# Kernel tuning notes

Hardware: AMD Instinct MI355X
Metric: run time of the kernel (lower is better)

Reference implementation:

```python
import jax, jax.numpy as jnp
import numpy as np

N_HEADS = 8
DIM = 128
BT, A, M = 2880, 10, 350  # bs*T, agents, map tokens (from forwards())
TOPK_SELF, TOPK_CROSS = 3, 32


def _split_heads(x, h):
    B, T, C = x.shape
    return x.reshape(B, T, h, C // h).transpose(0, 2, 1, 3)  # [B,h,T,hd]


def _biased_attn(q, k, v, pe, rel):
    """flex_attention with score_mod: score + pe[b,q,rel[b,q,kv],h], -inf where rel==-1.
    q:[B,H,Tq,d] k,v:[B,H,Tk,d] pe:[B,Tq,K,H] rel:[B,Tq,Tk] int"""
    d = q.shape[-1]
    scores = jnp.einsum('bhqd,bhkd->bhqk', q, k) / jnp.sqrt(jnp.asarray(d, q.dtype))
    safe = jnp.maximum(rel, 0)
    bias = jnp.take_along_axis(pe, safe[:, :, :, None], axis=2)  # [B,Tq,Tk,H]
    bias = bias.transpose(0, 3, 1, 2)                            # [B,H,Tq,Tk]
    scores = jnp.where(rel[:, None, :, :] > -1, scores + bias, -jnp.inf)
    attn = jax.nn.softmax(scores, axis=-1)
    out = jnp.einsum('bhqk,bhkd->bhqd', attn, v)
    B, H, Tq, hd = out.shape
    return out.transpose(0, 2, 1, 3).reshape(B, Tq, H * hd)


def _make_relation(key, B, Tq, Tk, topk):
    # topk random keys per query get offsets 0..topk-1 in ascending kv order; rest -1
    rand = jax.random.uniform(key, (B, Tq, Tk))
    idx = jnp.sort(jax.lax.top_k(rand, topk)[1], axis=-1)  # [B,Tq,topk]
    rel = jnp.full((B, Tq, Tk), -1, dtype=jnp.int32)
    b = jnp.arange(B)[:, None, None]
    qi = jnp.arange(Tq)[None, :, None]
    return rel.at[b, qi, idx].set(jnp.arange(topk, dtype=jnp.int32)[None, None, :])


def setup_inputs() -> dict:
    key = jax.random.key(0)
    ks = jax.random.split(key, 12)
    s = 0.02
    return {
        'a_token': jax.random.normal(ks[0], (BT, A, DIM), jnp.float32),
        'm_token': jax.random.normal(ks[1], (BT, M, DIM), jnp.float32),
        'a2m_pe': jax.random.uniform(ks[2], (BT, A, TOPK_CROSS, N_HEADS), jnp.float32),
        'a_pe': jax.random.uniform(ks[3], (BT, A, TOPK_SELF, N_HEADS), jnp.float32),
        'Wq': s * jax.random.normal(ks[4], (DIM, DIM), jnp.float32),
        'Wk': s * jax.random.normal(ks[5], (DIM, DIM), jnp.float32),
        'Wv': s * jax.random.normal(ks[6], (DIM, DIM), jnp.float32),
        'W_cross_proj': s * jax.random.normal(ks[7], (DIM, DIM), jnp.float32),
        'W_cattn': s * jax.random.normal(ks[8], (DIM, 3 * DIM), jnp.float32),
        'W_self_proj': s * jax.random.normal(ks[9], (DIM, DIM), jnp.float32),
        'a2m_relation': _make_relation(ks[10], BT, A, M, TOPK_CROSS),
        'a_relation': _make_relation(ks[11], BT, A, A, TOPK_SELF),
    }


def reference(a_token, m_token, a2m_pe, a_pe, Wq, Wk, Wv, W_cross_proj,
              W_cattn, W_self_proj, a2m_relation, a_relation):
    # cross attention: q from a_token, k/v from m_token (dropout=0 => identity)
    q = _split_heads(a_token @ Wq, N_HEADS)
    k = _split_heads(m_token @ Wk, N_HEADS)
    v = _split_heads(m_token @ Wv, N_HEADS)
    y = _biased_attn(q, k, v, a2m_pe, a2m_relation) @ W_cross_proj
    # self attention with fused qkv projection
    q2, k2, v2 = jnp.split(y @ W_cattn, 3, axis=-1)
    y2 = _biased_attn(_split_heads(q2, N_HEADS), _split_heads(k2, N_HEADS),
                      _split_heads(v2, N_HEADS), a_pe, a_relation)
    return y2 @ W_self_proj
```

## Files before the change

kernel.cpp:

```cpp
#include <hip/hip_runtime.h>
#include <hip/hip_bf16.h>


typedef __attribute__((ext_vector_type(4))) float f32x4;
typedef __attribute__((ext_vector_type(8))) short bf16x8v;
typedef __attribute__((ext_vector_type(4))) short short4v;

#define BT_N 2880
#define A_N  10
#define M_N  350
#define BQ_N (BT_N * A_N)
#define DIMC 128

static __device__ __forceinline__ short f2b(float x) {
    __hip_bfloat16 b = __float2bfloat16(x);
    return __builtin_bit_cast(short, b);
}
static __device__ __forceinline__ float b2f(short s) {
    unsigned u = ((unsigned)(unsigned short)s) << 16;
    return __builtin_bit_cast(float, u);
}

__global__ __launch_bounds__(256) void precompute_mats(
    const float* __restrict__ Wq, const float* __restrict__ Wk,
    const float* __restrict__ Wv, const float* __restrict__ Wcp,
    const float* __restrict__ Wc, const float* __restrict__ Wsp,
    short* __restrict__ S1t, short* __restrict__ VP1t,
    short* __restrict__ S2t, short* __restrict__ VP2t)
{
    int gid = blockIdx.x * 256 + threadIdx.x;
    int mat = gid >> 17;
    int idx = gid & 131071;
    float acc = 0.f;
    if (mat == 0) {
        int n = idx >> 7, c = idx & 127;
        int h = n >> 7, d = n & 127;
        #pragma unroll
        for (int t = 0; t < 16; ++t)
            acc += Wq[c * 128 + h * 16 + t] * Wk[d * 128 + h * 16 + t];
        S1t[idx] = f2b(acc * 0.25f);
    } else if (mat == 1) {
        int d = idx >> 10, o = idx & 1023;
        int h = o >> 7, c = o & 127;
        #pragma unroll
        for (int t = 0; t < 16; ++t)
            acc += Wv[c * 128 + h * 16 + t] * Wcp[(h * 16 + t) * 128 + d];
        VP1t[idx] = f2b(acc);
    } else if (mat == 2) {
        int n = idx >> 7, c = idx & 127;
        int h = n >> 7, d = n & 127;
        #pragma unroll
        for (int t = 0; t < 16; ++t)
            acc += Wc[c * 384 + h * 16 + t] * Wc[d * 384 + 128 + h * 16 + t];
        S2t[idx] = f2b(acc * 0.25f);
    } else {
        int d = idx >> 10, o = idx & 1023;
        int h = o >> 7, c = o & 127;
        #pragma unroll
        for (int t = 0; t < 16; ++t)
            acc += Wc[c * 384 + 256 + h * 16 + t] * Wsp[(h * 16 + t) * 128 + d];
        VP2t[idx] = f2b(acc);
    }
}

template<bool AF32, bool CF32>
__global__ __launch_bounds__(256) void gemm_bt(
    const void* __restrict__ Ap, const short* __restrict__ Bt,
    void* __restrict__ Cp, int M, int N, int K)
{
    __shared__ short As[128][72];
    __shared__ short Bs[128][72];
    const int tid  = threadIdx.x;
    const int bm   = blockIdx.y << 7, bn = blockIdx.x << 7;
    const int wave = tid >> 6, lane = tid & 63;
    const int wm   = (wave >> 1) << 6, wn = (wave & 1) << 6;
    const int row16 = lane & 15, kq = (lane >> 4) << 3;
    f32x4 acc[4][4] = {};

    for (int k0 = 0; k0 < K; k0 += 64) {
        if (AF32) {
            const float* A = (const float*)Ap;
            #pragma unroll
            for (int i = 0; i < 8; ++i) {
                int f = (i << 8) + tid;
                int r = f >> 4, c = (f & 15) << 2;
                f32x4 v = *(const f32x4*)(A + (size_t)(bm + r) * K + k0 + c);
                short4v t;
                t.x = f2b(v.x); t.y = f2b(v.y); t.z = f2b(v.z); t.w = f2b(v.w);
                *(short4v*)&As[r][c] = t;
            }
        } else {
            const short* A = (const short*)Ap;
            #pragma unroll
            for (int i = 0; i < 4; ++i) {
                int g = (i << 8) + tid;
                int r = g >> 3, c = (g & 7) << 3;
                *(bf16x8v*)&As[r][c] = *(const bf16x8v*)(A + (size_t)(bm + r) * K + k0 + c);
            }
        }
        #pragma unroll
        for (int i = 0; i < 4; ++i) {
            int g = (i << 8) + tid;
            int r = g >> 3, c = (g & 7) << 3;
            *(bf16x8v*)&Bs[r][c] = *(const bf16x8v*)(Bt + (size_t)(bn + r) * K + k0 + c);
        }
        __syncthreads();
        #pragma unroll
        for (int kk = 0; kk < 64; kk += 32) {
            bf16x8v af[4], bfr[4];
            #pragma unroll
            for (int mi = 0; mi < 4; ++mi)
                af[mi] = *(const bf16x8v*)&As[wm + (mi << 4) + row16][kq + kk];
            #pragma unroll
            for (int ni = 0; ni < 4; ++ni)
                bfr[ni] = *(const bf16x8v*)&Bs[wn + (ni << 4) + row16][kq + kk];
            #pragma unroll
            for (int mi = 0; mi < 4; ++mi)
                #pragma unroll
                for (int ni = 0; ni < 4; ++ni)
                    acc[mi][ni] = __builtin_amdgcn_mfma_f32_16x16x32_bf16(
                        af[mi], bfr[ni], acc[mi][ni], 0, 0, 0);
        }
        __syncthreads();
    }

    const int col = lane & 15, rb = (lane >> 4) << 2;
    #pragma unroll
    for (int mi = 0; mi < 4; ++mi)
        #pragma unroll
        for (int ni = 0; ni < 4; ++ni)
            #pragma unroll
            for (int r = 0; r < 4; ++r) {
                int rr = bm + wm + (mi << 4) + rb + r;
                int cc = bn + wn + (ni << 4) + col;
                float v = acc[mi][ni][r];
                if (CF32) ((float*)Cp)[(size_t)rr * N + cc] = v;
                else      ((short*)Cp)[(size_t)rr * N + cc] = f2b(v);
            }
}

__global__ __launch_bounds__(256) void attn_cross(
    const float* __restrict__ m_token, const short* __restrict__ qS,
    const float* __restrict__ pe, const int* __restrict__ rel,
    short* __restrict__ u)
{
    __shared__ float mrows[32][132];
    __shared__ float qsr[1024];
    __shared__ int   selk[32];
    __shared__ float wts[8][32];
    const int bq = blockIdx.x;
    const int b  = bq / A_N;
    const int tid = threadIdx.x;

    const int* relrow = rel + (size_t)bq * M_N;
    for (int k = tid; k < M_N; k += 256) {
        int r = relrow[k];
        if (r >= 0) selk[r] = k;
    }
    {
        short4v v = ((const short4v*)(qS + (size_t)bq * 1024))[tid];
        qsr[(tid << 2) + 0] = b2f(v.x);
        qsr[(tid << 2) + 1] = b2f(v.y);
        qsr[(tid << 2) + 2] = b2f(v.z);
        qsr[(tid << 2) + 3] = b2f(v.w);
    }
    __syncthreads();
    #pragma unroll
    for (int i = 0; i < 4; ++i) {
        int f = (i << 8) + tid;
        int r = f >> 5, c = (f & 31) << 2;
        f32x4 v = *(const f32x4*)(m_token + ((size_t)b * M_N + selk[r]) * DIMC + c);
        *(f32x4*)&mrows[r][c] = v;
    }
    __syncthreads();
    {
        const int h = tid >> 5, r = tid & 31;
        const float* qh = qsr + (h << 7);
        f32x4 p = {0.f, 0.f, 0.f, 0.f};
        #pragma unroll
        for (int d = 0; d < DIMC; d += 4)
            p += *(const f32x4*)(qh + d) * *(const f32x4*)&mrows[r][d];
        float sc = p.x + p.y + p.z + p.w + pe[((size_t)bq * 32 + r) * 8 + h];
        float mx = sc;
        #pragma unroll
        for (int off = 16; off; off >>= 1) mx = fmaxf(mx, __shfl_xor(mx, off, 32));
        float e = expf(sc - mx);
        float s = e;
        #pragma unroll
        for (int off = 16; off; off >>= 1) s += __shfl_xor(s, off, 32);
        wts[h][r] = e / s;
    }
    __syncthreads();
    {
        const int h = tid >> 5, d0 = (tid << 2) & 127;
        f32x4 acc = {0.f, 0.f, 0.f, 0.f};
        #pragma unroll
        for (int r = 0; r < 32; ++r)
            acc += wts[h][r] * *(const f32x4*)&mrows[r][d0];
        short4v t;
        t.x = f2b(acc.x); t.y = f2b(acc.y); t.z = f2b(acc.z); t.w = f2b(acc.w);
        *(short4v*)(u + (size_t)bq * 1024 + (tid << 2)) = t;
    }
}

__global__ __launch_bounds__(256) void attn_self(
    const short* __restrict__ ybf, const short* __restrict__ yS2,
    const float* __restrict__ pe, const int* __restrict__ rel,
    short* __restrict__ u2)
{
    __shared__ float yrows[3][132];
    __shared__ float ysr[1024];
    __shared__ int   selk[3];
    __shared__ float sw[8][3];
    const int bq = blockIdx.x;
    const int b  = bq / A_N;
    const int tid = threadIdx.x;

    if (tid < A_N) {
        int r = rel[(size_t)bq * A_N + tid];
        if (r >= 0) selk[r] = tid;
    }
    {
        short4v v = ((const short4v*)(yS2 + (size_t)bq * 1024))[tid];
        ysr[(tid << 2) + 0] = b2f(v.x);
        ysr[(tid << 2) + 1] = b2f(v.y);
        ysr[(tid << 2) + 2] = b2f(v.z);
        ysr[(tid << 2) + 3] = b2f(v.w);
    }
    __syncthreads();
    if (tid < 48) {
        int r = tid >> 4, c = (tid & 15) << 3;
        bf16x8v v = *(const bf16x8v*)(ybf + ((size_t)b * A_N + selk[r]) * DIMC + c);
        #pragma unroll
        for (int j = 0; j < 8; ++j) yrows[r][c + j] = b2f(v[j]);
    }
    __syncthreads();
    if (tid < 24) {
        int h = tid / 3, r = tid - h * 3;
        const float* qh = ysr + (h << 7);
        f32x4 p = {0.f, 0.f, 0.f, 0.f};
        #pragma unroll
        for (int d = 0; d < DIMC; d += 4)
            p += *(const f32x4*)(qh + d) * *(const f32x4*)&yrows[r][d];
        sw[h][r] = p.x + p.y + p.z + p.w + pe[((size_t)bq * 3 + r) * 8 + h];
    }
    __syncthreads();
    if (tid < 8) {
        float s0 = sw[tid][0], s1 = sw[tid][1], s2 = sw[tid][2];
        float mx = fmaxf(s0, fmaxf(s1, s2));
        float e0 = expf(s0 - mx), e1 = expf(s1 - mx), e2 = expf(s2 - mx);
        float inv = 1.f / (e0 + e1 + e2);
        sw[tid][0] = e0 * inv; sw[tid][1] = e1 * inv; sw[tid][2] = e2 * inv;
    }
    __syncthreads();
    {
        const int h = tid >> 5, d0 = (tid << 2) & 127;
        f32x4 acc = sw[h][0] * *(const f32x4*)&yrows[0][d0]
                  + sw[h][1] * *(const f32x4*)&yrows[1][d0]
                  + sw[h][2] * *(const f32x4*)&yrows[2][d0];
        short4v t;
        t.x = f2b(acc.x); t.y = f2b(acc.y); t.z = f2b(acc.z); t.w = f2b(acc.w);
        *(short4v*)(u2 + (size_t)bq * 1024 + (tid << 2)) = t;
    }
}

extern "C" void kernel_launch(void* const* d_in, const int* in_sizes, int n_in,
                              void* d_out, int out_size, void* d_ws, size_t ws_size,
                              hipStream_t stream)
{
    const float* a_token = (const float*)d_in[0];
    const float* m_token = (const float*)d_in[1];
    const float* a2m_pe  = (const float*)d_in[2];
    const float* a_pe    = (const float*)d_in[3];
    const float* Wq      = (const float*)d_in[4];
    const float* Wk      = (const float*)d_in[5];
    const float* Wv      = (const float*)d_in[6];
    const float* Wcp     = (const float*)d_in[7];
    const float* Wc      = (const float*)d_in[8];
    const float* Wsp     = (const float*)d_in[9];
    const int*   a2m_rel = (const int*)d_in[10];
    const int*   a_rel   = (const int*)d_in[11];

    char* ws = (char*)d_ws;
    short* S1t  = (short*)(ws + 0);
    short* VP1t = (short*)(ws + 262144);
    short* S2t  = (short*)(ws + 524288);
    short* VP2t = (short*)(ws + 786432);
    short* buf1 = (short*)(ws + 1048576);
    short* buf2 = (short*)(ws + 1048576 + 58982400ull);
    short* ybf  = (short*)(ws + 1048576 + 2ull * 58982400ull);
    float* outp = (float*)d_out;

    precompute_mats<<<dim3(2048), dim3(256), 0, stream>>>(
        Wq, Wk, Wv, Wcp, Wc, Wsp, S1t, VP1t, S2t, VP2t);

    gemm_bt<true, false><<<dim3(8, 225), dim3(256), 0, stream>>>(
        (const void*)a_token, S1t, (void*)buf1, BQ_N, 1024, 128);

    attn_cross<<<dim3(BQ_N), dim3(256), 0, stream>>>(
        m_token, buf1, a2m_pe, a2m_rel, buf2);

    gemm_bt<false, false><<<dim3(1, 225), dim3(256), 0, stream>>>(
        (const void*)buf2, VP1t, (void*)ybf, BQ_N, 128, 1024);

    gemm_bt<false, false><<<dim3(8, 225), dim3(256), 0, stream>>>(
        (const void*)ybf, S2t, (void*)buf1, BQ_N, 1024, 128);

    attn_self<<<dim3(BQ_N), dim3(256), 0, stream>>>(
        ybf, buf1, a_pe, a_rel, buf2);

    gemm_bt<false, true><<<dim3(1, 225), dim3(256), 0, stream>>>(
        (const void*)buf2, VP2t, (void*)outp, BQ_N, 128, 1024);
}
```

Baseline: 299.8 us.

## Pre-convert a_token to bf16, batch cross-attention per timestep, use fast exp

A separate kernel now converts a_token to bf16, so the first GEMM no longer repeats the fp32-to-bf16 conversion in each of its 8 column blocks. The cross-attention kernel launches one block per timestep and loops serially over its 10 agents, which gives L2/cache reuse of m_token rows and stages the bias into shared memory. The exp calls are replaced with __expf. The price is 10x fewer blocks (2880) with a serial loop and extra barriers, which lowers parallelism and latency hiding, plus one more kernel launch and an extra buffer round trip.

```diff
diff --git a/kernel.cpp b/kernel.cpp
--- a/kernel.cpp
+++ b/kernel.cpp
@@ -63,9 +63,21 @@
     }
 }
 
-template<bool AF32, bool CF32>
+__global__ __launch_bounds__(256) void conv_bf16(
+    const float* __restrict__ in, short* __restrict__ out)
+{
+    int i = blockIdx.x * 256 + threadIdx.x;
+    f32x4 a = ((const f32x4*)in)[2 * i];
+    f32x4 b = ((const f32x4*)in)[2 * i + 1];
+    bf16x8v t;
+    t[0] = f2b(a.x); t[1] = f2b(a.y); t[2] = f2b(a.z); t[3] = f2b(a.w);
+    t[4] = f2b(b.x); t[5] = f2b(b.y); t[6] = f2b(b.z); t[7] = f2b(b.w);
+    ((bf16x8v*)out)[i] = t;
+}
+
+template<bool CF32>
 __global__ __launch_bounds__(256) void gemm_bt(
-    const void* __restrict__ Ap, const short* __restrict__ Bt,
+    const short* __restrict__ Ap, const short* __restrict__ Bt,
     void* __restrict__ Cp, int M, int N, int K)
 {
     __shared__ short As[128][72];
@@ -78,25 +90,11 @@
     f32x4 acc[4][4] = {};
 
     for (int k0 = 0; k0 < K; k0 += 64) {
-        if (AF32) {
-            const float* A = (const float*)Ap;
-            #pragma unroll
-            for (int i = 0; i < 8; ++i) {
-                int f = (i << 8) + tid;
-                int r = f >> 4, c = (f & 15) << 2;
-                f32x4 v = *(const f32x4*)(A + (size_t)(bm + r) * K + k0 + c);
-                short4v t;
-                t.x = f2b(v.x); t.y = f2b(v.y); t.z = f2b(v.z); t.w = f2b(v.w);
-                *(short4v*)&As[r][c] = t;
-            }
-        } else {
-            const short* A = (const short*)Ap;
-            #pragma unroll
-            for (int i = 0; i < 4; ++i) {
-                int g = (i << 8) + tid;
-                int r = g >> 3, c = (g & 7) << 3;
-                *(bf16x8v*)&As[r][c] = *(const bf16x8v*)(A + (size_t)(bm + r) * K + k0 + c);
-            }
+        #pragma unroll
+        for (int i = 0; i < 4; ++i) {
+            int g = (i << 8) + tid;
+            int r = g >> 3, c = (g & 7) << 3;
+            *(bf16x8v*)&As[r][c] = *(const bf16x8v*)(Ap + (size_t)(bm + r) * K + k0 + c);
         }
         #pragma unroll
         for (int i = 0; i < 4; ++i) {
@@ -107,10 +105,10 @@
         __syncthreads();
         #pragma unroll
         for (int kk = 0; kk < 64; kk += 32) {
-            bf16x8v af[4], bfr[4];
+            bf16x8v afr[4], bfr[4];
             #pragma unroll
             for (int mi = 0; mi < 4; ++mi)
-                af[mi] = *(const bf16x8v*)&As[wm + (mi << 4) + row16][kq + kk];
+                afr[mi] = *(const bf16x8v*)&As[wm + (mi << 4) + row16][kq + kk];
             #pragma unroll
             for (int ni = 0; ni < 4; ++ni)
                 bfr[ni] = *(const bf16x8v*)&Bs[wn + (ni << 4) + row16][kq + kk];
@@ -119,7 +117,7 @@
                 #pragma unroll
                 for (int ni = 0; ni < 4; ++ni)
                     acc[mi][ni] = __builtin_amdgcn_mfma_f32_16x16x32_bf16(
-                        af[mi], bfr[ni], acc[mi][ni], 0, 0, 0);
+                        afr[mi], bfr[ni], acc[mi][ni], 0, 0, 0);
         }
         __syncthreads();
     }
@@ -139,7 +137,7 @@
             }
 }
 
-__global__ __launch_bounds__(256) void attn_cross(
+__global__ __launch_bounds__(256) void attn_cross_b(
     const float* __restrict__ m_token, const short* __restrict__ qS,
     const float* __restrict__ pe, const int* __restrict__ rel,
     short* __restrict__ u)
@@ -148,58 +146,63 @@
     __shared__ float qsr[1024];
     __shared__ int   selk[32];
     __shared__ float wts[8][32];
-    const int bq = blockIdx.x;
-    const int b  = bq / A_N;
+    __shared__ float peL[256];
+    const int b   = blockIdx.x;
     const int tid = threadIdx.x;
-
-    const int* relrow = rel + (size_t)bq * M_N;
-    for (int k = tid; k < M_N; k += 256) {
-        int r = relrow[k];
-        if (r >= 0) selk[r] = k;
-    }
-    {
-        short4v v = ((const short4v*)(qS + (size_t)bq * 1024))[tid];
-        qsr[(tid << 2) + 0] = b2f(v.x);
-        qsr[(tid << 2) + 1] = b2f(v.y);
-        qsr[(tid << 2) + 2] = b2f(v.z);
-        qsr[(tid << 2) + 3] = b2f(v.w);
-    }
-    __syncthreads();
-    #pragma unroll
-    for (int i = 0; i < 4; ++i) {
-        int f = (i << 8) + tid;
-        int r = f >> 5, c = (f & 31) << 2;
-        f32x4 v = *(const f32x4*)(m_token + ((size_t)b * M_N + selk[r]) * DIMC + c);
-        *(f32x4*)&mrows[r][c] = v;
-    }
-    __syncthreads();
-    {
-        const int h = tid >> 5, r = tid & 31;
-        const float* qh = qsr + (h << 7);
-        f32x4 p = {0.f, 0.f, 0.f, 0.f};
-        #pragma unroll
-        for (int d = 0; d < DIMC; d += 4)
-            p += *(const f32x4*)(qh + d) * *(const f32x4*)&mrows[r][d];
-        float sc = p.x + p.y + p.z + p.w + pe[((size_t)bq * 32 + r) * 8 + h];
-        float mx = sc;
-        #pragma unroll
-        for (int off = 16; off; off >>= 1) mx = fmaxf(mx, __shfl_xor(mx, off, 32));
-        float e = expf(sc - mx);
-        float s = e;
-        #pragma unroll
-        for (int off = 16; off; off >>= 1) s += __shfl_xor(s, off, 32);
-        wts[h][r] = e / s;
-    }
-    __syncthreads();
-    {
-        const int h = tid >> 5, d0 = (tid << 2) & 127;
-        f32x4 acc = {0.f, 0.f, 0.f, 0.f};
-        #pragma unroll
-        for (int r = 0; r < 32; ++r)
-            acc += wts[h][r] * *(const f32x4*)&mrows[r][d0];
-        short4v t;
-        t.x = f2b(acc.x); t.y = f2b(acc.y); t.z = f2b(acc.z); t.w = f2b(acc.w);
-        *(short4v*)(u + (size_t)bq * 1024 + (tid << 2)) = t;
+    const float* mb = m_token + (size_t)b * M_N * DIMC;
+
+    for (int q = 0; q < A_N; ++q) {
+        const int bq = b * A_N + q;
+        for (int k = tid; k < M_N; k += 256) {
+            int r = rel[(size_t)bq * M_N + k];
+            if (r >= 0) selk[r] = k;
+        }
+        {
+            short4v v = ((const short4v*)(qS + (size_t)bq * 1024))[tid];
+            qsr[(tid << 2) + 0] = b2f(v.x);
+            qsr[(tid << 2) + 1] = b2f(v.y);
+            qsr[(tid << 2) + 2] = b2f(v.z);
+            qsr[(tid << 2) + 3] = b2f(v.w);
+        }
+        peL[tid] = pe[(size_t)bq * 256 + tid];
+        __syncthreads();
+        #pragma unroll
+        for (int i = 0; i < 4; ++i) {
+            int f = (i << 8) + tid;
+            int r = f >> 5, c = (f & 31) << 2;
+            f32x4 v = *(const f32x4*)(mb + (size_t)selk[r] * DIMC + c);
+            *(f32x4*)&mrows[r][c] = v;
+        }
+        __syncthreads();
+        {
+            const int h = tid >> 5, r = tid & 31;
+            const float* qh = qsr + (h << 7);
+            f32x4 p = {0.f, 0.f, 0.f, 0.f};
+            #pragma unroll
+            for (int d = 0; d < DIMC; d += 4)
+                p += *(const f32x4*)(qh + d) * *(const f32x4*)&mrows[r][d];
+            float sc = p.x + p.y + p.z + p.w + peL[r * 8 + h];
+            float mx = sc;
+            #pragma unroll
+            for (int off = 16; off; off >>= 1) mx = fmaxf(mx, __shfl_xor(mx, off, 32));
+            float e = __expf(sc - mx);
+            float s = e;
+            #pragma unroll
+            for (int off = 16; off; off >>= 1) s += __shfl_xor(s, off, 32);
+            wts[h][r] = e / s;
+        }
+        __syncthreads();
+        {
+            const int h = tid >> 5, d0 = (tid << 2) & 127;
+            f32x4 acc = {0.f, 0.f, 0.f, 0.f};
+            #pragma unroll
+            for (int r = 0; r < 32; ++r)
+                acc += wts[h][r] * *(const f32x4*)&mrows[r][d0];
+            short4v t;
+            t.x = f2b(acc.x); t.y = f2b(acc.y); t.z = f2b(acc.z); t.w = f2b(acc.w);
+            *(short4v*)(u + (size_t)bq * 1024 + (tid << 2)) = t;
+        }
+        __syncthreads();
     }
 }
 
@@ -248,7 +251,7 @@
     if (tid < 8) {
         float s0 = sw[tid][0], s1 = sw[tid][1], s2 = sw[tid][2];
         float mx = fmaxf(s0, fmaxf(s1, s2));
-        float e0 = expf(s0 - mx), e1 = expf(s1 - mx), e2 = expf(s2 - mx);
+        float e0 = __expf(s0 - mx), e1 = __expf(s1 - mx), e2 = __expf(s2 - mx);
         float inv = 1.f / (e0 + e1 + e2);
         sw[tid][0] = e0 * inv; sw[tid][1] = e1 * inv; sw[tid][2] = e2 * inv;
     }
@@ -289,26 +292,29 @@
     short* buf1 = (short*)(ws + 1048576);
     short* buf2 = (short*)(ws + 1048576 + 58982400ull);
     short* ybf  = (short*)(ws + 1048576 + 2ull * 58982400ull);
+    short* abf  = (short*)(ws + 1048576 + 2ull * 58982400ull + 7372800ull);
     float* outp = (float*)d_out;
 
     precompute_mats<<<dim3(2048), dim3(256), 0, stream>>>(
         Wq, Wk, Wv, Wcp, Wc, Wsp, S1t, VP1t, S2t, VP2t);
 
-    gemm_bt<true, false><<<dim3(8, 225), dim3(256), 0, stream>>>(
-        (const void*)a_token, S1t, (void*)buf1, BQ_N, 1024, 128);
-
-    attn_cross<<<dim3(BQ_N), dim3(256), 0, stream>>>(
+    conv_bf16<<<dim3(1800), dim3(256), 0, stream>>>(a_token, abf);
+
+    gemm_bt<false><<<dim3(8, 225), dim3(256), 0, stream>>>(
+        abf, S1t, (void*)buf1, BQ_N, 1024, 128);
+
+    attn_cross_b<<<dim3(BT_N), dim3(256), 0, stream>>>(
         m_token, buf1, a2m_pe, a2m_rel, buf2);
 
-    gemm_bt<false, false><<<dim3(1, 225), dim3(256), 0, stream>>>(
-        (const void*)buf2, VP1t, (void*)ybf, BQ_N, 128, 1024);
-
-    gemm_bt<false, false><<<dim3(8, 225), dim3(256), 0, stream>>>(
-        (const void*)ybf, S2t, (void*)buf1, BQ_N, 1024, 128);
+    gemm_bt<false><<<dim3(1, 225), dim3(256), 0, stream>>>(
+        buf2, VP1t, (void*)ybf, BQ_N, 128, 1024);
+
+    gemm_bt<false><<<dim3(8, 225), dim3(256), 0, stream>>>(
+        ybf, S2t, (void*)buf1, BQ_N, 1024, 128);
 
     attn_self<<<dim3(BQ_N), dim3(256), 0, stream>>>(
         ybf, buf1, a_pe, a_rel, buf2);
 
-    gemm_bt<false, true><<<dim3(1, 225), dim3(256), 0, stream>>>(
-        (const void*)buf2, VP2t, (void*)outp, BQ_N, 128, 1024);
-}
+    gemm_bt<true><<<dim3(1, 225), dim3(256), 0, stream>>>(
+        buf2, VP2t, (void*)outp, BQ_N, 128, 1024);
+}
```

Result: slower. 319.6 us (+6.6%).
